# Kernel optimization log

Measured on AMD Instinct MI355X. Metric: run time of the kernel, lower is better.

Reference implementation:

```python
import jax, jax.numpy as jnp
import numpy as np

TEMPERATURE = 0.5


def setup_inputs() -> dict:
    key = jax.random.key(0)
    k1, k2 = jax.random.split(key)
    N, Z = 4096, 2048
    z1 = jax.random.normal(k1, (N, Z), dtype=jnp.float32)
    z2 = jax.random.normal(k2, (N, Z), dtype=jnp.float32)
    return {"z1": z1, "z2": z2}


def reference(z1, z2):
    # NT-Xent loss. Original torch code: normalize, build full 2Nx2N cosine-sim
    # matrix, prepend the positive pair column, cross-entropy with label 0.
    # Mathematically, per-row CE with the positive prepended and the self-sim
    # removed equals: logsumexp over the row excluding the diagonal, minus the
    # positive logit.  (cosine_similarity on already-normalized vectors is a
    # plain dot product, so normalization is applied once.)
    n, _ = z1.shape
    a = z1 / jnp.linalg.norm(z1, axis=1, keepdims=True)  # [N, Z]
    b = z2 / jnp.linalg.norm(z2, axis=1, keepdims=True)  # [N, Z]
    reps = jnp.concatenate([a, b], axis=0)               # [2N, Z]
    logits = jnp.matmul(reps, reps.T) / TEMPERATURE      # [2N, 2N]
    NEG_INF = jnp.float32(-1e9)  # mask self-similarity (excluded from CE denom)
    logits = jnp.where(jnp.eye(2 * n, dtype=bool), NEG_INF, logits)
    pos = jnp.sum(a * b, axis=1) / TEMPERATURE           # [N] positive logits
    pos = jnp.concatenate([pos, pos])                    # [2N]
    lse = jax.nn.logsumexp(logits, axis=1)               # [2N]
    # sum of CE over 2N rows, divided by 2N  == mean
    return jnp.mean(lse - pos)
```

## Files before the change

### kernel.cpp

```cpp
#include <hip/hip_runtime.h>
#include <stdint.h>

#define N_ROWS 4096
#define Z_DIM  2048
#define TOT    8192
#define TILE   128
#define RBYTES (Z_DIM / 2)
#define BKE    128
#define KBYT   (BKE / 2)
#define NITER  (Z_DIM / BKE)
#define NT     (TOT / TILE)
#define NBLK   (NT * (NT + 1) / 2)
#define INV_T  2.0f
#define SCL4   64.0f

typedef __attribute__((ext_vector_type(4))) int   intx4;
typedef __attribute__((ext_vector_type(8))) int   intx8;
typedef __attribute__((ext_vector_type(4))) float floatx4;

#define GLOAD16(g, l)                                                   \
    __builtin_amdgcn_global_load_lds(                                   \
        (const __attribute__((address_space(1))) unsigned int*)(g),     \
        (__attribute__((address_space(3))) unsigned int*)(l), 16, 0, 0)

__device__ __forceinline__ unsigned int f2fp4(float v) {
    float a = fabsf(v);
    unsigned int c = (a >= 0.25f) + (a >= 0.75f) + (a >= 1.25f) + (a >= 1.75f)
                   + (a >= 2.5f)  + (a >= 3.5f)  + (a >= 5.0f);
    return c | (v < 0.f ? 8u : 0u);
}

__global__ __launch_bounds__(256) void normalize_kernel(
    const float* __restrict__ z1, const float* __restrict__ z2,
    unsigned char* __restrict__ reps, float* __restrict__ pos,
    float* __restrict__ rowsum)
{
    const int row  = blockIdx.x;
    const int tid  = threadIdx.x;
    const int lane = tid & 63, wave = tid >> 6;

    if (row < TOT / 256) rowsum[row * 256 + tid] = 0.f;

    const float4* p1 = (const float4*)(z1 + (size_t)row * Z_DIM);
    const float4* p2 = (const float4*)(z2 + (size_t)row * Z_DIM);
    float4 x0 = p1[tid * 2], x1 = p1[tid * 2 + 1];
    float4 y0 = p2[tid * 2], y1 = p2[tid * 2 + 1];

    float s1 = x0.x*x0.x + x0.y*x0.y + x0.z*x0.z + x0.w*x0.w
             + x1.x*x1.x + x1.y*x1.y + x1.z*x1.z + x1.w*x1.w;
    float s2 = y0.x*y0.x + y0.y*y0.y + y0.z*y0.z + y0.w*y0.w
             + y1.x*y1.x + y1.y*y1.y + y1.z*y1.z + y1.w*y1.w;
    float dd = x0.x*y0.x + x0.y*y0.y + x0.z*y0.z + x0.w*y0.w
             + x1.x*y1.x + x1.y*y1.y + x1.z*y1.z + x1.w*y1.w;

    #pragma unroll
    for (int m = 1; m < 64; m <<= 1) {
        s1 += __shfl_xor(s1, m);
        s2 += __shfl_xor(s2, m);
        dd += __shfl_xor(dd, m);
    }
    __shared__ float red[3][4];
    if (lane == 0) { red[0][wave] = s1; red[1][wave] = s2; red[2][wave] = dd; }
    __syncthreads();
    s1 = red[0][0] + red[0][1] + red[0][2] + red[0][3];
    s2 = red[1][0] + red[1][1] + red[1][2] + red[1][3];
    dd = red[2][0] + red[2][1] + red[2][2] + red[2][3];

    const float inv1 = rsqrtf(s1), inv2 = rsqrtf(s2);
    if (tid == 0) {
        float p = dd * inv1 * inv2 * INV_T;
        pos[row] = p;
        pos[row + N_ROWS] = p;
    }

    const float a = inv1 * SCL4, b = inv2 * SCL4;
    unsigned int pa =  f2fp4(x0.x * a)        | (f2fp4(x0.y * a) << 4)
                    | (f2fp4(x0.z * a) << 8)  | (f2fp4(x0.w * a) << 12)
                    | (f2fp4(x1.x * a) << 16) | (f2fp4(x1.y * a) << 20)
                    | (f2fp4(x1.z * a) << 24) | (f2fp4(x1.w * a) << 28);
    unsigned int pb =  f2fp4(y0.x * b)        | (f2fp4(y0.y * b) << 4)
                    | (f2fp4(y0.z * b) << 8)  | (f2fp4(y0.w * b) << 12)
                    | (f2fp4(y1.x * b) << 16) | (f2fp4(y1.y * b) << 20)
                    | (f2fp4(y1.z * b) << 24) | (f2fp4(y1.w * b) << 28);
    *(unsigned int*)(reps + (size_t)row * RBYTES + tid * 4) = pa;
    *(unsigned int*)(reps + (size_t)(N_ROWS + row) * RBYTES + tid * 4) = pb;
}

__global__ __launch_bounds__(256) void simclr_gemm(
    const unsigned char* __restrict__ reps, float* __restrict__ rowsum)
{
    __shared__ __align__(16) unsigned char L[2][2][TILE * KBYT];

    const int t = blockIdx.x;
    int r = (int)((sqrtf(8.0f * (float)t + 1.0f) - 1.0f) * 0.5f);
    while ((r + 1) * (r + 2) / 2 <= t) ++r;
    while (r * (r + 1) / 2 > t) --r;
    const int bi = t - r * (r + 1) / 2;
    const int bj = r;
    const bool diag = (bi == bj);

    const int tid  = threadIdx.x;
    const int lane = tid & 63, wave = tid >> 6;
    const int wr = wave >> 1, wc = wave & 1;
    const int quad = lane >> 4, l16 = lane & 15;
    const int sw   = l16 & 3;
    const int row0 = bi * TILE, col0 = bj * TILE;

    floatx4 acc[4][4];
    #pragma unroll
    for (int i = 0; i < 4; ++i)
        #pragma unroll
        for (int j = 0; j < 4; ++j)
            acc[i][j] = floatx4{0.f, 0.f, 0.f, 0.f};

    const int c0 = tid, c1 = tid + 256;
    const int r0s = c0 >> 2, k0s = (c0 & 3) ^ (r0s & 3);
    const int r1s = c1 >> 2, k1s = (c1 & 3) ^ (r1s & 3);
    const unsigned char* gA0 = reps + (size_t)(row0 + r0s) * RBYTES + k0s * 16;
    const unsigned char* gA1 = reps + (size_t)(row0 + r1s) * RBYTES + k1s * 16;
    const unsigned char* gB0 = reps + (size_t)(col0 + r0s) * RBYTES + k0s * 16;
    const unsigned char* gB1 = reps + (size_t)(col0 + r1s) * RBYTES + k1s * 16;
    const int o0 = c0 * 16, o1 = c1 * 16;

    GLOAD16(gA0, &L[0][0][o0]);
    GLOAD16(gA1, &L[0][0][o1]);
    GLOAD16(gB0, &L[0][1][o0]);
    GLOAD16(gB1, &L[0][1][o1]);
    __syncthreads();

    for (int i = 0; i < NITER; ++i) {
        if (i + 1 < NITER) {
            const size_t ko = (size_t)(i + 1) * KBYT;
            const int buf = (i + 1) & 1;
            GLOAD16(gA0 + ko, &L[buf][0][o0]);
            GLOAD16(gA1 + ko, &L[buf][0][o1]);
            GLOAD16(gB0 + ko, &L[buf][1][o0]);
            GLOAD16(gB1 + ko, &L[buf][1][o1]);
        }
        const unsigned char* Ab = &L[i & 1][0][0];
        const unsigned char* Bb = &L[i & 1][1][0];

        intx8 af[4], bf[4];
        #pragma unroll
        for (int fi = 0; fi < 4; ++fi) {
            const int ar = (wr * 64 + fi * 16 + l16) * KBYT;
            const int br = (wc * 64 + fi * 16 + l16) * KBYT;
            intx4 av = *(const intx4*)&Ab[ar + ((quad ^ sw) << 4)];
            intx4 bv = *(const intx4*)&Bb[br + ((quad ^ sw) << 4)];
            af[fi] = intx8{av[0], av[1], av[2], av[3], 0, 0, 0, 0};
            bf[fi] = intx8{bv[0], bv[1], bv[2], bv[3], 0, 0, 0, 0};
        }
        #pragma unroll
        for (int fi = 0; fi < 4; ++fi)
            #pragma unroll
            for (int j = 0; j < 4; ++j)
                acc[fi][j] = __builtin_amdgcn_mfma_scale_f32_16x16x128_f8f6f4(
                    af[fi], bf[j], acc[fi][j],
                    4, 4,
                    0, 0x7F7F7F7Fu,
                    0, 0x7F7F7F7Fu);
        __syncthreads();
    }

    const float descale = INV_T / (SCL4 * SCL4);
    float scol[4] = {0.f, 0.f, 0.f, 0.f};
    #pragma unroll
    for (int fi = 0; fi < 4; ++fi) {
        const int rbase = row0 + wr * 64 + fi * 16 + quad * 4;
        float srow[4] = {0.f, 0.f, 0.f, 0.f};
        #pragma unroll
        for (int j = 0; j < 4; ++j) {
            const int c = col0 + wc * 64 + j * 16 + l16;
            #pragma unroll
            for (int rr = 0; rr < 4; ++rr) {
                float e = __expf(acc[fi][j][rr] * descale);
                if (diag && (rbase + rr == c)) e = 0.f;
                srow[rr] += e;
                scol[j]  += e;
            }
        }
        #pragma unroll
        for (int rr = 0; rr < 4; ++rr) {
            #pragma unroll
            for (int m = 1; m < 16; m <<= 1) srow[rr] += __shfl_xor(srow[rr], m);
        }
        if (l16 == 0) {
            #pragma unroll
            for (int rr = 0; rr < 4; ++rr)
                atomicAdd(&rowsum[rbase + rr], srow[rr]);
        }
    }
    if (!diag) {
        #pragma unroll
        for (int j = 0; j < 4; ++j) {
            scol[j] += __shfl_xor(scol[j], 16);
            scol[j] += __shfl_xor(scol[j], 32);
        }
        if (quad == 0) {
            #pragma unroll
            for (int j = 0; j < 4; ++j)
                atomicAdd(&rowsum[col0 + wc * 64 + j * 16 + l16], scol[j]);
        }
    }
}

__global__ __launch_bounds__(1024) void finalize_kernel(
    const float* __restrict__ rowsum, const float* __restrict__ pos,
    float* __restrict__ out)
{
    const int tid = threadIdx.x;
    const int lane = tid & 63, wave = tid >> 6;
    float s = 0.f;
    for (int r = tid; r < TOT; r += 1024) s += logf(rowsum[r]) - pos[r];
    #pragma unroll
    for (int m = 1; m < 64; m <<= 1) s += __shfl_xor(s, m);
    __shared__ float red[16];
    if (lane == 0) red[wave] = s;
    __syncthreads();
    if (tid == 0) {
        float t = 0.f;
        #pragma unroll
        for (int w = 0; w < 16; ++w) t += red[w];
        out[0] = t * (1.0f / TOT);
    }
}

extern "C" void kernel_launch(void* const* d_in, const int* in_sizes, int n_in,
                              void* d_out, int out_size, void* d_ws, size_t ws_size,
                              hipStream_t stream)
{
    const float* z1 = (const float*)d_in[0];
    const float* z2 = (const float*)d_in[1];
    float* out = (float*)d_out;

    char* w = (char*)d_ws;
    unsigned char* reps = (unsigned char*)w;
    float* pos    = (float*)(w + (size_t)TOT * RBYTES);
    float* rowsum = pos + TOT;

    normalize_kernel<<<N_ROWS, 256, 0, stream>>>(z1, z2, reps, pos, rowsum);
    simclr_gemm<<<NBLK, 256, 0, stream>>>(reps, rowsum);
    finalize_kernel<<<1, 1024, 0, stream>>>(rowsum, pos, out);
}
```

Measured before the change: 159.5 us.

## Use 256x128 triangular tiles with triple-buffered async LDS pipeline

Enlarges GEMM blocks to 256x128 over the upper triangle. Replaces double buffering with a three-stage global-to-LDS pipeline driven by explicit vmcnt waits and raw barriers. Diagonal handling moves to a strict upper-triangular mask, with idle waves skipped on diagonal tiles, and MFMA issue priority is raised. The goals are better operand reuse, deeper latency hiding and fewer per-iteration syncs. In exchange it drops the LDS XOR swizzle, which may cause bank conflicts, and it raises register pressure with the 8x4 accumulator array.

```diff
diff --git a/kernel.cpp b/kernel.cpp
--- a/kernel.cpp
+++ b/kernel.cpp
@@ -4,13 +4,15 @@
 #define N_ROWS 4096
 #define Z_DIM  2048
 #define TOT    8192
-#define TILE   128
 #define RBYTES (Z_DIM / 2)
 #define BKE    128
 #define KBYT   (BKE / 2)
 #define NITER  (Z_DIM / BKE)
-#define NT     (TOT / TILE)
-#define NBLK   (NT * (NT + 1) / 2)
+#define BM     256
+#define BN     128
+#define NBLK   1056
+#define ABYTES (BM * KBYT)
+#define BUFB   (ABYTES + BN * KBYT)
 #define INV_T  2.0f
 #define SCL4   64.0f
 
@@ -86,111 +88,125 @@
     *(unsigned int*)(reps + (size_t)(N_ROWS + row) * RBYTES + tid * 4) = pb;
 }
 
-__global__ __launch_bounds__(256) void simclr_gemm(
+__global__ __launch_bounds__(256, 2) void simclr_gemm(
     const unsigned char* __restrict__ reps, float* __restrict__ rowsum)
 {
-    __shared__ __align__(16) unsigned char L[2][2][TILE * KBYT];
+    __shared__ __align__(16) unsigned char L[3 * BUFB];
 
     const int t = blockIdx.x;
-    int r = (int)((sqrtf(8.0f * (float)t + 1.0f) - 1.0f) * 0.5f);
-    while ((r + 1) * (r + 2) / 2 <= t) ++r;
-    while (r * (r + 1) / 2 > t) --r;
-    const int bi = t - r * (r + 1) / 2;
-    const int bj = r;
-    const bool diag = (bi == bj);
+    int ri = (int)((65.0f - sqrtf(4225.0f - 4.0f * (float)t)) * 0.5f);
+    while (ri * (65 - ri) > t) --ri;
+    while ((ri + 1) * (64 - ri) <= t) ++ri;
+    const int cj = 2 * ri + (t - ri * (65 - ri));
+
+    const int row0 = ri * BM;
+    const int col0 = cj * BN;
 
     const int tid  = threadIdx.x;
     const int lane = tid & 63, wave = tid >> 6;
     const int wr = wave >> 1, wc = wave & 1;
     const int quad = lane >> 4, l16 = lane & 15;
-    const int sw   = l16 & 3;
-    const int row0 = bi * TILE, col0 = bj * TILE;
-
-    floatx4 acc[4][4];
-    #pragma unroll
-    for (int i = 0; i < 4; ++i)
+
+    const bool deadW = (cj == 2 * ri) && (wr == 1);
+
+    const unsigned char* gsrc[6];
+    int lofs[6];
+    #pragma unroll
+    for (int c = 0; c < 6; ++c) {
+        const int m   = wave * 384 + c * 64 + lane;
+        const int opB = (m >= ABYTES / 16);
+        const int mm  = opB ? m - ABYTES / 16 : m;
+        const int gr  = (opB ? col0 : row0) + (mm >> 2);
+        gsrc[c] = reps + (size_t)gr * RBYTES + (mm & 3) * 16;
+        lofs[c] = m * 16;
+    }
+
+    floatx4 acc[8][4];
+    #pragma unroll
+    for (int i = 0; i < 8; ++i)
         #pragma unroll
         for (int j = 0; j < 4; ++j)
             acc[i][j] = floatx4{0.f, 0.f, 0.f, 0.f};
 
-    const int c0 = tid, c1 = tid + 256;
-    const int r0s = c0 >> 2, k0s = (c0 & 3) ^ (r0s & 3);
-    const int r1s = c1 >> 2, k1s = (c1 & 3) ^ (r1s & 3);
-    const unsigned char* gA0 = reps + (size_t)(row0 + r0s) * RBYTES + k0s * 16;
-    const unsigned char* gA1 = reps + (size_t)(row0 + r1s) * RBYTES + k1s * 16;
-    const unsigned char* gB0 = reps + (size_t)(col0 + r0s) * RBYTES + k0s * 16;
-    const unsigned char* gB1 = reps + (size_t)(col0 + r1s) * RBYTES + k1s * 16;
-    const int o0 = c0 * 16, o1 = c1 * 16;
-
-    GLOAD16(gA0, &L[0][0][o0]);
-    GLOAD16(gA1, &L[0][0][o1]);
-    GLOAD16(gB0, &L[0][1][o0]);
-    GLOAD16(gB1, &L[0][1][o1]);
-    __syncthreads();
-
+    #pragma unroll
+    for (int c = 0; c < 6; ++c) GLOAD16(gsrc[c],        &L[lofs[c]]);
+    #pragma unroll
+    for (int c = 0; c < 6; ++c) GLOAD16(gsrc[c] + KBYT, &L[BUFB + lofs[c]]);
+
+    int cur = 0;
+    #pragma unroll 1
     for (int i = 0; i < NITER; ++i) {
-        if (i + 1 < NITER) {
-            const size_t ko = (size_t)(i + 1) * KBYT;
-            const int buf = (i + 1) & 1;
-            GLOAD16(gA0 + ko, &L[buf][0][o0]);
-            GLOAD16(gA1 + ko, &L[buf][0][o1]);
-            GLOAD16(gB0 + ko, &L[buf][1][o0]);
-            GLOAD16(gB1 + ko, &L[buf][1][o1]);
-        }
-        const unsigned char* Ab = &L[i & 1][0][0];
-        const unsigned char* Bb = &L[i & 1][1][0];
-
-        intx8 af[4], bf[4];
-        #pragma unroll
-        for (int fi = 0; fi < 4; ++fi) {
-            const int ar = (wr * 64 + fi * 16 + l16) * KBYT;
-            const int br = (wc * 64 + fi * 16 + l16) * KBYT;
-            intx4 av = *(const intx4*)&Ab[ar + ((quad ^ sw) << 4)];
-            intx4 bv = *(const intx4*)&Bb[br + ((quad ^ sw) << 4)];
-            af[fi] = intx8{av[0], av[1], av[2], av[3], 0, 0, 0, 0};
-            bf[fi] = intx8{bv[0], bv[1], bv[2], bv[3], 0, 0, 0, 0};
-        }
-        #pragma unroll
-        for (int fi = 0; fi < 4; ++fi)
-            #pragma unroll
-            for (int j = 0; j < 4; ++j)
-                acc[fi][j] = __builtin_amdgcn_mfma_scale_f32_16x16x128_f8f6f4(
-                    af[fi], bf[j], acc[fi][j],
-                    4, 4,
-                    0, 0x7F7F7F7Fu,
-                    0, 0x7F7F7F7Fu);
-        __syncthreads();
+        if (i + 1 < NITER) asm volatile("s_waitcnt vmcnt(6)" ::: "memory");
+        else               asm volatile("s_waitcnt vmcnt(0)" ::: "memory");
+        __builtin_amdgcn_s_barrier();
+        asm volatile("" ::: "memory");
+
+        if (i + 2 < NITER) {
+            int pf = cur + 2; if (pf >= 3) pf -= 3;
+            unsigned char* Lp = &L[pf * BUFB];
+            const int ko = (i + 2) * KBYT;
+            #pragma unroll
+            for (int c = 0; c < 6; ++c) GLOAD16(gsrc[c] + ko, Lp + lofs[c]);
+        }
+
+        if (!deadW) {
+            const unsigned char* Lc = &L[cur * BUFB];
+            intx8 b8[4];
+            #pragma unroll
+            for (int j = 0; j < 4; ++j) {
+                intx4 bv = *(const intx4*)(Lc + ABYTES
+                             + (wc * 64 + j * 16 + l16) * KBYT + quad * 16);
+                b8[j] = intx8{bv[0], bv[1], bv[2], bv[3], 0, 0, 0, 0};
+            }
+            #pragma unroll
+            for (int fi = 0; fi < 8; ++fi) {
+                intx4 av = *(const intx4*)(Lc
+                             + (wr * 128 + fi * 16 + l16) * KBYT + quad * 16);
+                intx8 a8 = intx8{av[0], av[1], av[2], av[3], 0, 0, 0, 0};
+                __builtin_amdgcn_s_setprio(1);
+                #pragma unroll
+                for (int j = 0; j < 4; ++j)
+                    acc[fi][j] = __builtin_amdgcn_mfma_scale_f32_16x16x128_f8f6f4(
+                        a8, b8[j], acc[fi][j],
+                        4, 4,
+                        0, 0x7F7F7F7Fu,
+                        0, 0x7F7F7F7Fu);
+                __builtin_amdgcn_s_setprio(0);
+            }
+        }
+        cur = (cur == 2) ? 0 : cur + 1;
     }
 
     const float descale = INV_T / (SCL4 * SCL4);
-    float scol[4] = {0.f, 0.f, 0.f, 0.f};
-    #pragma unroll
-    for (int fi = 0; fi < 4; ++fi) {
-        const int rbase = row0 + wr * 64 + fi * 16 + quad * 4;
-        float srow[4] = {0.f, 0.f, 0.f, 0.f};
-        #pragma unroll
-        for (int j = 0; j < 4; ++j) {
-            const int c = col0 + wc * 64 + j * 16 + l16;
+    if (!deadW) {
+        float scol[4] = {0.f, 0.f, 0.f, 0.f};
+        #pragma unroll
+        for (int fi = 0; fi < 8; ++fi) {
+            const int rbase = row0 + wr * 128 + fi * 16 + quad * 4;
+            float srow[4] = {0.f, 0.f, 0.f, 0.f};
+            #pragma unroll
+            for (int j = 0; j < 4; ++j) {
+                const int c = col0 + wc * 64 + j * 16 + l16;
+                #pragma unroll
+                for (int rr = 0; rr < 4; ++rr) {
+                    float e = (c > rbase + rr)
+                            ? __expf(acc[fi][j][rr] * descale) : 0.f;
+                    srow[rr] += e;
+                    scol[j]  += e;
+                }
+            }
             #pragma unroll
             for (int rr = 0; rr < 4; ++rr) {
-                float e = __expf(acc[fi][j][rr] * descale);
-                if (diag && (rbase + rr == c)) e = 0.f;
-                srow[rr] += e;
-                scol[j]  += e;
-            }
-        }
-        #pragma unroll
-        for (int rr = 0; rr < 4; ++rr) {
-            #pragma unroll
-            for (int m = 1; m < 16; m <<= 1) srow[rr] += __shfl_xor(srow[rr], m);
-        }
-        if (l16 == 0) {
-            #pragma unroll
-            for (int rr = 0; rr < 4; ++rr)
-                atomicAdd(&rowsum[rbase + rr], srow[rr]);
-        }
-    }
-    if (!diag) {
+                #pragma unroll
+                for (int m = 1; m < 16; m <<= 1)
+                    srow[rr] += __shfl_xor(srow[rr], m);
+            }
+            if (l16 == 0) {
+                #pragma unroll
+                for (int rr = 0; rr < 4; ++rr)
+                    atomicAdd(&rowsum[rbase + rr], srow[rr]);
+            }
+        }
         #pragma unroll
         for (int j = 0; j < 4; ++j) {
             scol[j] += __shfl_xor(scol[j], 16);
```

Result: slower. 170.5 us (+6.9%).
